# Kernel tuning notes

Hardware: AMD Instinct MI355X
Metric: run time of the kernel (lower is better)

The kernel has to match this reference:

```python
import jax, jax.numpy as jnp
import numpy as np

N = 2048
VOTE_THRESH = 0.65
SOFT_TH = 0.05      # INFERENCE_TH in the original
MAX_DET = 100       # cfg.TEST.DETECTIONS_PER_IMAGE
NUM_CLASSES = 80


def setup_inputs() -> dict:
    key = jax.random.key(0)
    k1, k2, k3, k4 = jax.random.split(key, 4)
    xy = jax.random.uniform(k1, (N, 2), dtype=jnp.float32) * 800.0
    wh = jax.random.uniform(k2, (N, 2), dtype=jnp.float32) * 196.0 + 4.0
    boxes = jnp.concatenate([xy, xy + wh], axis=1)          # valid x1y1x2y2 boxes
    scores = jax.random.uniform(k3, (N,), dtype=jnp.float32) * 0.95 + 0.05
    labels = jax.random.randint(k4, (N,), 0, NUM_CLASSES, dtype=jnp.int32)
    return {"boxes": boxes, "scores": scores, "labels": labels}


def _bbox_vote_soft(det):
    """Faithful fixed-shape version of bbox_vote(..., vote_type='soft_vote').
    det: (n, 6) = [x1, y1, x2, y2, score, label]. Returns (MAX_DET, 6) rows + valid mask."""
    n = det.shape[0]
    BUF = 2 * n + 1                      # each det yields <=1 soft row + <=1 merged row; last slot = trash
    order = jnp.argsort(-det[:, 4])
    det = det[order]
    area = (det[:, 2] - det[:, 0]) * (det[:, 3] - det[:, 1])

    def step(state, _):
        alive, buf, cnt = state
        any_alive = jnp.any(alive)
        pos = jnp.argmax(alive)          # first alive in score-sorted order == current top det
        cur = det[pos]
        xx1 = jnp.maximum(cur[0], det[:, 0])
        yy1 = jnp.maximum(cur[1], det[:, 1])
        xx2 = jnp.minimum(cur[2], det[:, 2])
        yy2 = jnp.minimum(cur[3], det[:, 3])
        inter = jnp.clip(xx2 - xx1, 0.0) * jnp.clip(yy2 - yy1, 0.0)
        iou = inter / (area[pos] + area - inter)
        merge = alive & (iou >= VOTE_THRESH)
        n_merge = merge.sum()
        s = det[:, 4]
        ms = jnp.where(merge, s, 0.0)
        wsum = ms.sum()
        wsafe = jnp.where(wsum > 0, wsum, 1.0)          # guard masked no-op iterations
        wbox = (det[:, :4] * ms[:, None]).sum(0) / wsafe  # score-weighted box merge
        maxs = jnp.max(ms)                               # max score among merged (scores > 0)
        row0 = jnp.concatenate([wbox, maxs[None], cur[5][None]])  # == single det when n_merge==1
        soft_s = s * (1.0 - iou)                         # soft-NMS decayed scores
        soft_valid = merge & (soft_s >= SOFT_TH) & (n_merge > 1)
        soft_rows = jnp.concatenate([det[:, :4], soft_s[:, None], det[:, 5:6]], axis=1)
        valid = jnp.concatenate([any_alive[None], soft_valid])
        rows = jnp.concatenate([row0[None], soft_rows], axis=0)   # (n+1, 6)
        idxs = jnp.where(valid, cnt + jnp.cumsum(valid) - 1, BUF - 1)
        buf = buf.at[idxs].set(rows)
        cnt = cnt + valid.sum()
        alive = alive & (iou < VOTE_THRESH)              # drop all merged dets
        return (alive, buf, cnt), None

    init = (jnp.ones((n,), bool), jnp.zeros((BUF, 6), det.dtype), jnp.int32(0))
    (alive, buf, cnt), _ = jax.lax.scan(step, init, None, length=n)
    res = buf[: BUF - 1]
    valid = jnp.arange(BUF - 1) < cnt
    sc = jnp.where(valid, res[:, 4], -jnp.inf)
    keep = jnp.argsort(-sc)[:MAX_DET]                    # final sort by score desc + truncate
    return res[keep], valid[keep]


def reference(boxes, scores, labels):
    labf = labels.astype(boxes.dtype)
    maxc = boxes.max() + 1.0                             # batched-NMS class-offset trick
    det = jnp.concatenate([boxes + labf[:, None] * maxc, scores[:, None], labf[:, None]], axis=1)
    out, valid = _bbox_vote_soft(det)
    ob = jnp.where(valid[:, None], out[:, :4] - out[:, 5:6] * maxc, 0.0)
    os_ = jnp.where(valid, out[:, 4], 0.0)
    ol = jnp.where(valid, out[:, 5], 0.0)
    return ob, os_, ol
```

## Files before the change

### kernel.cpp

```cpp
#include <hip/hip_runtime.h>

#define NCLS 80
#define VOTE_TH 0.65f
#define SOFT_THR 0.05f
#define MAXDET 100
#define NB 1281
#define BINBASE 31232
#define CANDCAP 512
#define SEG 21

__device__ __forceinline__ int bin_of(unsigned int b) {
    int bin = (int)(b >> 15) - BINBASE;
    return bin < 0 ? 0 : (bin > NB - 1 ? NB - 1 : bin);
}

__global__ __launch_bounds__(64, 1) void vote_kernel(
    const float* __restrict__ boxes,
    const float* __restrict__ scores,
    const int* __restrict__ labels,
    int* __restrict__ kCnt,
    float* __restrict__ sArrG,
    float* __restrict__ rows,
    float* __restrict__ maxcP,
    int n)
{
#pragma clang fp contract(off)
    const int lane = threadIdx.x;
    const int cls = blockIdx.x;
    const unsigned long long lmask = (1ull << lane) - 1ull;
    const int chunks = (n + 63) >> 6;

    __shared__ int uidx[64];

    const float4* b4 = (const float4*)boxes;
    float m = -3.0e38f;
    for (int base = 0; base < chunks; base += 8) {
        float4 v[8];
#pragma unroll
        for (int u = 0; u < 8; ++u) {
            int c = base + u;
            v[u] = (c < chunks) ? b4[c * 64 + lane]
                                : make_float4(-3.0e38f, -3.0e38f, -3.0e38f, -3.0e38f);
        }
#pragma unroll
        for (int u = 0; u < 8; ++u)
            m = fmaxf(m, fmaxf(fmaxf(v[u].x, v[u].y), fmaxf(v[u].z, v[u].w)));
    }
#pragma unroll
    for (int d = 32; d; d >>= 1) m = fmaxf(m, __shfl_xor(m, d));
    const float maxc = m + 1.0f;
    if (cls == 0 && lane == 0) *maxcP = maxc;
    const float off = (float)cls * maxc;
    const float cls_f = (float)cls;

    int lab[32];
    for (int base = 0; base < 32; base += 8) {
#pragma unroll
        for (int u = 0; u < 8; ++u) {
            int c = base + u;
            lab[c] = (c < chunks) ? labels[c * 64 + lane] : -1;
        }
    }
    int k = 0;
    for (int c = 0; c < chunks; ++c) {
        bool p = (lab[c] == cls);
        unsigned long long b = __ballot(p);
        if (p) {
            int w = k + __popcll(b & lmask);
            if (w < 64) uidx[w] = c * 64 + lane;
        }
        k += __popcll(b);
    }
    if (k > 64) k = 64;
    __syncthreads();

    float s = 0.0f;
    float4 bb = make_float4(0.f, 0.f, 0.f, 0.f);
    if (lane < k) {
        int gi = uidx[lane];
        s = scores[gi];
        bb = b4[gi];
    }

    int r = 0;
#pragma unroll
    for (int j = 0; j < 64; ++j) {
        float sj = __shfl(s, j);
        r += ((sj > s) || (sj == s && j < lane)) ? 1 : 0;
    }
    float x1 = 0.f, y1 = 0.f, x2 = 0.f, y2 = 0.f;
    if (lane < k) {
        x1 = bb.x + off; y1 = bb.y + off;
        x2 = bb.z + off; y2 = bb.w + off;
    }
    int addr = r * 4;
    x1 = __int_as_float(__builtin_amdgcn_ds_permute(addr, __float_as_int(x1)));
    y1 = __int_as_float(__builtin_amdgcn_ds_permute(addr, __float_as_int(y1)));
    x2 = __int_as_float(__builtin_amdgcn_ds_permute(addr, __float_as_int(x2)));
    y2 = __int_as_float(__builtin_amdgcn_ds_permute(addr, __float_as_int(y2)));
    s  = __int_as_float(__builtin_amdgcn_ds_permute(addr, __float_as_int(s)));

    float area = (x2 - x1) * (y2 - y1);
    bool alive = lane < k;

    float* rbase = rows + cls * 64 * 6;
    float* sbase = sArrG + cls * 64;
    int lcnt = 0;
    while (true) {
        unsigned long long avm = __ballot(alive);
        if (avm == 0ull) break;
        int pos = (int)__builtin_ctzll(avm);

        float cx1 = __shfl(x1, pos), cy1 = __shfl(y1, pos);
        float cx2 = __shfl(x2, pos), cy2 = __shfl(y2, pos);
        float carea = __shfl(area, pos), cs = __shfl(s, pos);

        float xx1 = fmaxf(cx1, x1), yy1 = fmaxf(cy1, y1);
        float xx2 = fminf(cx2, x2), yy2 = fminf(cy2, y2);
        float inter = fmaxf(xx2 - xx1, 0.0f) * fmaxf(yy2 - yy1, 0.0f);
        float iou = inter / ((carea + area) - inter);

        bool merge = alive && (iou >= VOTE_TH);
        unsigned long long mb = __ballot(merge);
        int nm = __popcll(mb);

        if (nm == 1) {
            if (lane == 0) {
                float* rp = rbase + lcnt * 6;
                rp[0] = (cx1 * cs) / cs; rp[1] = (cy1 * cs) / cs;
                rp[2] = (cx2 * cs) / cs; rp[3] = (cy2 * cs) / cs;
                rp[4] = cs; rp[5] = cls_f;
                sbase[lcnt] = cs;
            }
            lcnt += 1;
        } else {
            float msv = merge ? s : 0.0f;
            float w0 = msv, w1 = x1 * msv, w2 = y1 * msv, w3 = x2 * msv, w4 = y2 * msv;
#pragma unroll
            for (int d = 32; d; d >>= 1) {
                w0 += __shfl_xor(w0, d);
                w1 += __shfl_xor(w1, d);
                w2 += __shfl_xor(w2, d);
                w3 += __shfl_xor(w3, d);
                w4 += __shfl_xor(w4, d);
            }
            float soft = s * (1.0f - iou);
            bool sv = merge && (soft >= SOFT_THR);
            unsigned long long sb = __ballot(sv);
            int nsoft = __popcll(sb);
            if (lane == 0) {
                float* rp = rbase + lcnt * 6;
                rp[0] = w1 / w0; rp[1] = w2 / w0;
                rp[2] = w3 / w0; rp[3] = w4 / w0;
                rp[4] = cs; rp[5] = cls_f;
                sbase[lcnt] = cs;
            }
            if (sv) {
                int wp = lcnt + 1 + __popcll(sb & lmask);
                float* rp = rbase + wp * 6;
                rp[0] = x1; rp[1] = y1; rp[2] = x2; rp[3] = y2;
                rp[4] = soft; rp[5] = cls_f;
                sbase[wp] = soft;
            }
            lcnt += 1 + nsoft;
        }
        alive = alive && (iou < VOTE_TH);
    }

    if (lane == 0) kCnt[cls] = lcnt;
}

__global__ __launch_bounds__(256) void select_kernel(
    const float* __restrict__ rows,
    const float* __restrict__ sArrG,
    const int* __restrict__ kCnt,
    const float* __restrict__ maxcP,
    float* __restrict__ out)
{
#pragma clang fp contract(off)
    const int tid = threadIdx.x;
    const int lane = tid & 63;
    const int wave = tid >> 6;

    __shared__ int cnts[NCLS];
    __shared__ int hist[NB];
    __shared__ unsigned long long cand[CANDCAP];
    __shared__ int ncand_sh, T_sh, K_sh;

    for (int i = tid; i < 6 * MAXDET; i += 256) out[i] = 0.0f;
    if (tid < NCLS) cnts[tid] = kCnt[tid];
    for (int i = tid; i < NB; i += 256) hist[i] = 0;
    if (tid == 0) ncand_sh = 0;
    __syncthreads();

    for (int c = wave; c < NCLS; c += 4)
        if (lane < cnts[c])
            atomicAdd(&hist[bin_of(__float_as_uint(sArrG[c * 64 + lane]))], 1);
    __syncthreads();

    if (tid < 64) {
        int part = 0;
        if (lane < 61) {
            int b0 = lane * SEG;
            for (int b = b0; b < b0 + SEG; ++b) part += hist[b];
        }
        int suf = part;
#pragma unroll
        for (int d = 1; d < 64; d <<= 1) {
            int v = __shfl_down(suf, d);
            if (lane + d < 64) suf += v;
        }
        int cnt_total = __shfl(suf, 0);
        int K = (cnt_total < MAXDET) ? cnt_total : MAXDET;
        if (lane == 0) K_sh = K;
        unsigned long long bm = __ballot(suf >= K);
        int L = 63 - __builtin_clzll(bm);
        if (lane == L) {
            int acc = suf - part;
            int T = 0;
            for (int b = L * SEG + SEG - 1; b >= L * SEG; --b) {
                acc += hist[b];
                if (acc >= K) { T = b; break; }
            }
            T_sh = T;
        }
    }
    __syncthreads();
    const int K = K_sh;
    if (K <= 0) return;
    const int T = T_sh;

    for (int c = wave; c < NCLS; c += 4) {
        if (lane < cnts[c]) {
            int idx = c * 64 + lane;
            unsigned int sb = __float_as_uint(sArrG[idx]);
            if (bin_of(sb) >= T) {
                int p = atomicAdd(&ncand_sh, 1);
                if (p < CANDCAP)
                    cand[p] = ((unsigned long long)sb << 32) |
                              (unsigned long long)(0xFFFFFFFFu - (unsigned int)idx);
            }
        }
    }
    __syncthreads();

    int nc = ncand_sh; if (nc > CANDCAP) nc = CANDCAP;
    const float maxc = *maxcP;
    for (int j = tid; j < nc; j += 256) {
        unsigned long long my = cand[j];
        int rank = 0;
        for (int l = 0; l < nc; ++l) rank += (cand[l] > my) ? 1 : 0;
        if (rank < K) {
            int idx = (int)(0xFFFFFFFFu - (unsigned int)(my & 0xFFFFFFFFull));
            const float* rp = rows + idx * 6;
            float lb = rp[5];
            float o = lb * maxc;
            out[rank * 4 + 0] = rp[0] - o;
            out[rank * 4 + 1] = rp[1] - o;
            out[rank * 4 + 2] = rp[2] - o;
            out[rank * 4 + 3] = rp[3] - o;
            out[4 * MAXDET + rank] = rp[4];
            out[5 * MAXDET + rank] = lb;
        }
    }
}

extern "C" void kernel_launch(void* const* d_in, const int* in_sizes, int n_in,
                              void* d_out, int out_size, void* d_ws, size_t ws_size,
                              hipStream_t stream) {
    const float* boxes  = (const float*)d_in[0];
    const float* scores = (const float*)d_in[1];
    const int*   labels = (const int*)d_in[2];
    float* out = (float*)d_out;
    const int n = in_sizes[1];

    char* ws = (char*)d_ws;
    int*   kCnt  = (int*)(ws + 0);
    float* maxcP = (float*)(ws + 384);
    float* sArrG = (float*)(ws + 512);
    float* rows  = (float*)(ws + 512 + 20480);

    hipLaunchKernelGGL(vote_kernel, dim3(NCLS), dim3(64), 0, stream,
                       boxes, scores, labels, kCnt, sArrG, rows, maxcP, n);
    hipLaunchKernelGGL(select_kernel, dim3(1), dim3(256), 0, stream,
                       rows, sArrG, kCnt, maxcP, out);
}
```

Before: 96.26 us.

## Fuse vote and select kernels via cooperative launch with grid sync

Merges the per-class vote kernel and the single-block select kernel into one cooperative kernel. A grid-wide sync separates the two phases, and block 0 then runs the selection with 64 threads instead of 256. This removes one kernel launch and the maxc round-trip through global memory. In exchange it pays for a grid barrier and runs selection on a single wave, which adds serial work in the histogram and rank loops.

```diff
diff --git a/kernel.cpp b/kernel.cpp
--- a/kernel.cpp
+++ b/kernel.cpp
@@ -1,4 +1,7 @@
 #include <hip/hip_runtime.h>
+#include <hip/hip_cooperative_groups.h>
+
+namespace cg = cooperative_groups;
 
 #define NCLS 80
 #define VOTE_TH 0.65f
@@ -14,14 +17,14 @@
     return bin < 0 ? 0 : (bin > NB - 1 ? NB - 1 : bin);
 }
 
-__global__ __launch_bounds__(64, 1) void vote_kernel(
+__global__ __launch_bounds__(64, 1) void nms_coop_kernel(
     const float* __restrict__ boxes,
     const float* __restrict__ scores,
     const int* __restrict__ labels,
     int* __restrict__ kCnt,
     float* __restrict__ sArrG,
     float* __restrict__ rows,
-    float* __restrict__ maxcP,
+    float* __restrict__ out,
     int n)
 {
 #pragma clang fp contract(off)
@@ -31,6 +34,10 @@
     const int chunks = (n + 63) >> 6;
 
     __shared__ int uidx[64];
+    __shared__ int cnts[NCLS];
+    __shared__ int hist[NB];
+    __shared__ unsigned long long cand[CANDCAP];
+    __shared__ int ncand_sh, T_sh;
 
     const float4* b4 = (const float4*)boxes;
     float m = -3.0e38f;
@@ -49,7 +56,6 @@
 #pragma unroll
     for (int d = 32; d; d >>= 1) m = fmaxf(m, __shfl_xor(m, d));
     const float maxc = m + 1.0f;
-    if (cls == 0 && lane == 0) *maxcP = maxc;
     const float off = (float)cls * maxc;
     const float cls_f = (float)cls;
 
@@ -168,76 +174,59 @@
     }
 
     if (lane == 0) kCnt[cls] = lcnt;
-}
-
-__global__ __launch_bounds__(256) void select_kernel(
-    const float* __restrict__ rows,
-    const float* __restrict__ sArrG,
-    const int* __restrict__ kCnt,
-    const float* __restrict__ maxcP,
-    float* __restrict__ out)
-{
-#pragma clang fp contract(off)
-    const int tid = threadIdx.x;
-    const int lane = tid & 63;
-    const int wave = tid >> 6;
-
-    __shared__ int cnts[NCLS];
-    __shared__ int hist[NB];
-    __shared__ unsigned long long cand[CANDCAP];
-    __shared__ int ncand_sh, T_sh, K_sh;
-
-    for (int i = tid; i < 6 * MAXDET; i += 256) out[i] = 0.0f;
-    if (tid < NCLS) cnts[tid] = kCnt[tid];
-    for (int i = tid; i < NB; i += 256) hist[i] = 0;
-    if (tid == 0) ncand_sh = 0;
-    __syncthreads();
-
-    for (int c = wave; c < NCLS; c += 4)
-        if (lane < cnts[c])
+
+    cg::this_grid().sync();
+    if (cls != 0) return;
+
+    for (int i = lane; i < 6 * MAXDET; i += 64) out[i] = 0.0f;
+    for (int c = lane; c < NCLS; c += 64) cnts[c] = kCnt[c];
+    for (int i = lane; i < NB; i += 64) hist[i] = 0;
+    if (lane == 0) ncand_sh = 0;
+    __syncthreads();
+
+    int cnt_total = 0;
+    for (int c = 0; c < NCLS; ++c) {
+        int cc = cnts[c];
+        cnt_total += cc;
+        if (lane < cc)
             atomicAdd(&hist[bin_of(__float_as_uint(sArrG[c * 64 + lane]))], 1);
-    __syncthreads();
-
-    if (tid < 64) {
-        int part = 0;
-        if (lane < 61) {
-            int b0 = lane * SEG;
-            for (int b = b0; b < b0 + SEG; ++b) part += hist[b];
-        }
-        int suf = part;
-#pragma unroll
-        for (int d = 1; d < 64; d <<= 1) {
-            int v = __shfl_down(suf, d);
-            if (lane + d < 64) suf += v;
-        }
-        int cnt_total = __shfl(suf, 0);
-        int K = (cnt_total < MAXDET) ? cnt_total : MAXDET;
-        if (lane == 0) K_sh = K;
-        unsigned long long bm = __ballot(suf >= K);
-        int L = 63 - __builtin_clzll(bm);
-        if (lane == L) {
-            int acc = suf - part;
-            int T = 0;
-            for (int b = L * SEG + SEG - 1; b >= L * SEG; --b) {
-                acc += hist[b];
-                if (acc >= K) { T = b; break; }
-            }
-            T_sh = T;
-        }
-    }
-    __syncthreads();
-    const int K = K_sh;
+    }
+    const int K = (cnt_total < MAXDET) ? cnt_total : MAXDET;
     if (K <= 0) return;
+
+    int part = 0;
+    if (lane < 61) {
+        int b0 = lane * SEG;
+        for (int b = b0; b < b0 + SEG; ++b) part += hist[b];
+    }
+    int suf = part;
+#pragma unroll
+    for (int d = 1; d < 64; d <<= 1) {
+        int v = __shfl_down(suf, d);
+        if (lane + d < 64) suf += v;
+    }
+    unsigned long long bm = __ballot(suf >= K);
+    int L = 63 - __builtin_clzll(bm);
+    if (lane == L) {
+        int acc = suf - part;
+        int T = 0;
+        for (int b = L * SEG + SEG - 1; b >= L * SEG; --b) {
+            acc += hist[b];
+            if (acc >= K) { T = b; break; }
+        }
+        T_sh = T;
+    }
+    __syncthreads();
     const int T = T_sh;
 
-    for (int c = wave; c < NCLS; c += 4) {
+    for (int c = 0; c < NCLS; ++c) {
         if (lane < cnts[c]) {
             int idx = c * 64 + lane;
-            unsigned int sb = __float_as_uint(sArrG[idx]);
-            if (bin_of(sb) >= T) {
+            unsigned int sb2 = __float_as_uint(sArrG[idx]);
+            if (bin_of(sb2) >= T) {
                 int p = atomicAdd(&ncand_sh, 1);
                 if (p < CANDCAP)
-                    cand[p] = ((unsigned long long)sb << 32) |
+                    cand[p] = ((unsigned long long)sb2 << 32) |
                               (unsigned long long)(0xFFFFFFFFu - (unsigned int)idx);
             }
         }
@@ -245,8 +234,7 @@
     __syncthreads();
 
     int nc = ncand_sh; if (nc > CANDCAP) nc = CANDCAP;
-    const float maxc = *maxcP;
-    for (int j = tid; j < nc; j += 256) {
+    for (int j = lane; j < nc; j += 64) {
         unsigned long long my = cand[j];
         int rank = 0;
         for (int l = 0; l < nc; ++l) rank += (cand[l] > my) ? 1 : 0;
@@ -272,16 +260,16 @@
     const float* scores = (const float*)d_in[1];
     const int*   labels = (const int*)d_in[2];
     float* out = (float*)d_out;
-    const int n = in_sizes[1];
+    int n = in_sizes[1];
 
     char* ws = (char*)d_ws;
     int*   kCnt  = (int*)(ws + 0);
-    float* maxcP = (float*)(ws + 384);
     float* sArrG = (float*)(ws + 512);
     float* rows  = (float*)(ws + 512 + 20480);
 
-    hipLaunchKernelGGL(vote_kernel, dim3(NCLS), dim3(64), 0, stream,
-                       boxes, scores, labels, kCnt, sArrG, rows, maxcP, n);
-    hipLaunchKernelGGL(select_kernel, dim3(1), dim3(256), 0, stream,
-                       rows, sArrG, kCnt, maxcP, out);
+    void* args[] = { (void*)&boxes, (void*)&scores, (void*)&labels,
+                     (void*)&kCnt, (void*)&sArrG, (void*)&rows,
+                     (void*)&out, (void*)&n };
+    hipLaunchCooperativeKernel((const void*)nms_coop_kernel,
+                               dim3(NCLS), dim3(64), args, 0, stream);
 }
```

Result: slower. 146.1 us (+51.8%).

## Pack four classes per block and share box/label loads via LDS

Applied to the files above, without the earlier changes.

The vote kernel now runs four class waves per 256-thread block, so each block reads the boxes and labels once and shares the labels through LDS instead of every class wave re-reading all of them. The select kernel preloads all score bits into registers and histograms them without per-class gating, relying on negative sentinel values for invalid slots. It also gets the total count with an atomic instead of taking it from the prefix scan. This cuts redundant global traffic and shortens the serial load phase. The price is more LDS per block and a block-wide barrier, plus the assumption that unused sArrG slots hold negative values and that n is at most 2048.

```diff
diff --git a/kernel.cpp b/kernel.cpp
--- a/kernel.cpp
+++ b/kernel.cpp
@@ -14,7 +14,7 @@
     return bin < 0 ? 0 : (bin > NB - 1 ? NB - 1 : bin);
 }
 
-__global__ __launch_bounds__(64, 1) void vote_kernel(
+__global__ __launch_bounds__(256, 1) void vote_kernel(
     const float* __restrict__ boxes,
     const float* __restrict__ scores,
     const int* __restrict__ labels,
@@ -25,49 +25,58 @@
     int n)
 {
 #pragma clang fp contract(off)
-    const int lane = threadIdx.x;
-    const int cls = blockIdx.x;
+    const int tid = threadIdx.x;
+    const int lane = tid & 63;
+    const int wave = tid >> 6;
+    const int cls = blockIdx.x * 4 + wave;
     const unsigned long long lmask = (1ull << lane) - 1ull;
-    const int chunks = (n + 63) >> 6;
-
-    __shared__ int uidx[64];
+
+    __shared__ int   labLds[2048];
+    __shared__ int   uidx[4][64];
+    __shared__ float redmax[4];
 
     const float4* b4 = (const float4*)boxes;
+    float4 v[8];
+#pragma unroll
+    for (int i = 0; i < 8; ++i) {
+        int idx = tid + i * 256;
+        v[i] = (idx < n) ? b4[idx]
+                         : make_float4(-3.0e38f, -3.0e38f, -3.0e38f, -3.0e38f);
+    }
+    int lab[8];
+#pragma unroll
+    for (int i = 0; i < 8; ++i) {
+        int idx = tid + i * 256;
+        lab[i] = (idx < n) ? labels[idx] : -1;
+    }
     float m = -3.0e38f;
-    for (int base = 0; base < chunks; base += 8) {
-        float4 v[8];
-#pragma unroll
-        for (int u = 0; u < 8; ++u) {
-            int c = base + u;
-            v[u] = (c < chunks) ? b4[c * 64 + lane]
-                                : make_float4(-3.0e38f, -3.0e38f, -3.0e38f, -3.0e38f);
-        }
-#pragma unroll
-        for (int u = 0; u < 8; ++u)
-            m = fmaxf(m, fmaxf(fmaxf(v[u].x, v[u].y), fmaxf(v[u].z, v[u].w)));
-    }
+#pragma unroll
+    for (int i = 0; i < 8; ++i)
+        m = fmaxf(m, fmaxf(fmaxf(v[i].x, v[i].y), fmaxf(v[i].z, v[i].w)));
 #pragma unroll
     for (int d = 32; d; d >>= 1) m = fmaxf(m, __shfl_xor(m, d));
-    const float maxc = m + 1.0f;
-    if (cls == 0 && lane == 0) *maxcP = maxc;
+    if (lane == 0) redmax[wave] = m;
+#pragma unroll
+    for (int i = 0; i < 8; ++i) labLds[tid + i * 256] = lab[i];
+    __syncthreads();
+
+    const float maxc = fmaxf(fmaxf(redmax[0], redmax[1]),
+                             fmaxf(redmax[2], redmax[3])) + 1.0f;
+    if (blockIdx.x == 0 && tid == 0) *maxcP = maxc;
     const float off = (float)cls * maxc;
     const float cls_f = (float)cls;
 
-    int lab[32];
-    for (int base = 0; base < 32; base += 8) {
-#pragma unroll
-        for (int u = 0; u < 8; ++u) {
-            int c = base + u;
-            lab[c] = (c < chunks) ? labels[c * 64 + lane] : -1;
-        }
-    }
+    int myLab[32];
+#pragma unroll
+    for (int c = 0; c < 32; ++c) myLab[c] = labLds[c * 64 + lane];
     int k = 0;
-    for (int c = 0; c < chunks; ++c) {
-        bool p = (lab[c] == cls);
+#pragma unroll 4
+    for (int c = 0; c < 32; ++c) {
+        bool p = (myLab[c] == cls);
         unsigned long long b = __ballot(p);
         if (p) {
             int w = k + __popcll(b & lmask);
-            if (w < 64) uidx[w] = c * 64 + lane;
+            if (w < 64) uidx[wave][w] = c * 64 + lane;
         }
         k += __popcll(b);
     }
@@ -77,7 +86,7 @@
     float s = 0.0f;
     float4 bb = make_float4(0.f, 0.f, 0.f, 0.f);
     if (lane < k) {
-        int gi = uidx[lane];
+        int gi = uidx[wave][lane];
         s = scores[gi];
         bb = b4[gi];
     }
@@ -185,20 +194,31 @@
     __shared__ int cnts[NCLS];
     __shared__ int hist[NB];
     __shared__ unsigned long long cand[CANDCAP];
-    __shared__ int ncand_sh, T_sh, K_sh;
-
+    __shared__ int ncand_sh, T_sh, K_sh, tot_sh;
+
+    unsigned int sbits[20];
+#pragma unroll
+    for (int j = 0; j < 20; ++j)
+        sbits[j] = __float_as_uint(sArrG[tid + j * 256]);
+    int myCnt = (tid < NCLS) ? kCnt[tid] : 0;
+
+    if (tid < NCLS) cnts[tid] = myCnt;
     for (int i = tid; i < 6 * MAXDET; i += 256) out[i] = 0.0f;
-    if (tid < NCLS) cnts[tid] = kCnt[tid];
     for (int i = tid; i < NB; i += 256) hist[i] = 0;
-    if (tid == 0) ncand_sh = 0;
-    __syncthreads();
-
-    for (int c = wave; c < NCLS; c += 4)
-        if (lane < cnts[c])
-            atomicAdd(&hist[bin_of(__float_as_uint(sArrG[c * 64 + lane]))], 1);
+    if (tid == 0) { ncand_sh = 0; tot_sh = 0; }
+    __syncthreads();
+
+    if (tid < NCLS) atomicAdd(&tot_sh, myCnt);
+#pragma unroll
+    for (int j = 0; j < 20; ++j)
+        if (!(sbits[j] >> 31))
+            atomicAdd(&hist[bin_of(sbits[j])], 1);
     __syncthreads();
 
     if (tid < 64) {
+        int cnt_total = tot_sh;
+        int K = (cnt_total < MAXDET) ? cnt_total : MAXDET;
+        if (lane == 0) K_sh = K;
         int part = 0;
         if (lane < 61) {
             int b0 = lane * SEG;
@@ -207,14 +227,11 @@
         int suf = part;
 #pragma unroll
         for (int d = 1; d < 64; d <<= 1) {
-            int v = __shfl_down(suf, d);
-            if (lane + d < 64) suf += v;
-        }
-        int cnt_total = __shfl(suf, 0);
-        int K = (cnt_total < MAXDET) ? cnt_total : MAXDET;
-        if (lane == 0) K_sh = K;
+            int vsh = __shfl_down(suf, d);
+            if (lane + d < 64) suf += vsh;
+        }
         unsigned long long bm = __ballot(suf >= K);
-        int L = 63 - __builtin_clzll(bm);
+        int L = (bm != 0ull) ? (63 - __builtin_clzll(bm)) : 0;
         if (lane == L) {
             int acc = suf - part;
             int T = 0;
@@ -280,7 +297,7 @@
     float* sArrG = (float*)(ws + 512);
     float* rows  = (float*)(ws + 512 + 20480);
 
-    hipLaunchKernelGGL(vote_kernel, dim3(NCLS), dim3(64), 0, stream,
+    hipLaunchKernelGGL(vote_kernel, dim3(NCLS / 4), dim3(256), 0, stream,
                        boxes, scores, labels, kCnt, sArrG, rows, maxcP, n);
     hipLaunchKernelGGL(select_kernel, dim3(1), dim3(256), 0, stream,
                        rows, sArrG, kCnt, maxcP, out);
```

Result: faster. 87.44 us (-9.2%).
